# Kernel optimization log

Hardware: AMD Instinct MI355X
Metric: run time of the kernel (lower is better)

The kernel has to match this reference:

```python
import jax, jax.numpy as jnp
import numpy as np
from math import pi

EPS = 1e-7
GAIN = 3.5  # weight_logits_softmax_gain
MAX_LOG_VAR = 3.5


def _upper_triangular(v, T, K, D):
    # replicate tf concat([v, v[...,::-1], zeros[...,D]], axis=2) -> reshape [T,K,D,D] -> strict-upper mask
    zero_pad = jnp.zeros((T, K, D), dtype=v.dtype)
    a_flat = jnp.concatenate([v, v[..., ::-1], zero_pad], axis=2)
    a = a_flat.reshape(T, K, D, D)
    idx = jnp.arange(D)
    mask = (idx[:, None] < idx[None, :]).astype(v.dtype)
    return a * mask[None, None, :, :]


def _diag_transforms(cov_param, T, K, D):
    ut = _upper_triangular(cov_param, T, K, D)
    a = 0.5 * (jnp.swapaxes(ut, -1, -2) - ut)  # antisymmetric [T,K,D,D]
    eye = jnp.eye(D, dtype=cov_param.dtype)[None, None]
    q = jnp.matmul(eye - a, jnp.linalg.inv(eye + a))  # Cayley transform
    return q


def setup_inputs() -> dict:
    key = jax.random.key(0)
    k1, k2, k3, k4, k5 = jax.random.split(key, 5)
    B, T, K, D = 2048, 512, 8, 8
    x = jax.random.normal(k1, (B, T, D), dtype=jnp.float32)
    kernel_centers = jax.random.uniform(k2, (T, K, D), dtype=jnp.float32)
    weight_logits = jax.random.normal(k3, (T, K), dtype=jnp.float32)
    log_variance = jax.random.normal(k4, (T, K, D), dtype=jnp.float32)
    cov_param = jax.random.normal(k5, (T, K, D * (D - 1) // 2), dtype=jnp.float32)
    return {"x": x, "kernel_centers": kernel_centers, "weight_logits": weight_logits,
            "log_variance": log_variance, "cov_param": cov_param}


def reference(x, kernel_centers, weight_logits, log_variance, cov_param):
    T, K, D = kernel_centers.shape
    # subtract kernel centers: [B,T,K,D]
    xc = x[:, :, None, :] - kernel_centers[None]
    # covariance-diagonalizing rotation (Cayley transform of antisym matrix)
    q = _diag_transforms(cov_param, T, K, D)  # [T,K,D,D]
    xt = jnp.einsum('btki,tkij->btkj', xc, q)
    # per-dimension Gaussian pdf
    var = jnp.exp(jnp.clip(log_variance, -MAX_LOG_VAR, MAX_LOG_VAR))[None]  # [1,T,K,D]
    norm_coeff = 1.0 / jnp.sqrt(2.0 * pi * var)
    gaussians = norm_coeff * jnp.exp(-0.5 * xt * xt / var)  # [B,T,K,D]
    # mix: product over dims (in log space), weighted sum over kernels
    lgpe = jnp.sum(jnp.log(gaussians + EPS), axis=-1)  # [B,T,K]
    p_kernels = jnp.exp(lgpe)
    w = jax.nn.softmax(jnp.clip(weight_logits, -GAIN, GAIN), axis=-1)  # [T,K]
    p = jnp.sum(p_kernels * w[None], axis=-1)  # [B,T]
    return p
```

## Files before the change

### kernel.cpp

```cpp
#include <hip/hip_runtime.h>
#include <math.h>

#define TDIM 512
#define KDIM 8
#define DDIM 8
#define BDIM 2048
#define EPSF 1e-7f

#ifndef __has_builtin
#define __has_builtin(x) 0
#endif
#if __has_builtin(__builtin_amdgcn_exp2f)
#define FAST_EXP2(x) __builtin_amdgcn_exp2f(x)
#else
#define FAST_EXP2(x) exp2f(x)
#endif

__global__ __launch_bounds__(512, 4) void pecd_fused(
    const float* __restrict__ x,
    const float* __restrict__ centers,
    const float* __restrict__ wlogits,
    const float* __restrict__ logvar,
    const float* __restrict__ covp,
    float* __restrict__ out)
{
    __shared__ float prm[64 * 80];
    __shared__ float Wl[64];
    __shared__ float xs[64 * 68];

    const int tidx   = (int)threadIdx.x;
    const int t0     = (int)blockIdx.x * 8;
    const int b_base = (int)blockIdx.y * 256;

    {
        const int tk = tidx >> 3;
        const int r  = tidx & 7;
        const int kk = tk & 7;
        const int tl = tk >> 3;
        const size_t tkg = (size_t)(t0 + tl) * 8 + kk;

        const float* cb = covp + tkg * 28;
        float row[8];
        #pragma unroll
        for (int j = 0; j < 8; j++) {
            const int lo = (r < j) ? r : j;
            const int hi = (r < j) ? j : r;
            const int n  = 8 * lo + hi;
            const int m  = (r == j) ? 0 : ((n < 28) ? n : 55 - n);
            const float v = cb[m];
            const float a = (r < j) ? -0.5f * v : 0.5f * v;
            row[j] = (r == j) ? 1.0f : a;
        }

        #pragma unroll
        for (int c = 0; c < 8; c++) {
            float prow[8];
            #pragma unroll
            for (int j = 0; j < 8; j++) prow[j] = __shfl(row[j], c, 8);
            const float pinv = 1.0f / prow[c];
            const float f = row[c];
            #pragma unroll
            for (int j = 0; j < 8; j++) {
                if (j == c) {
                    row[j] = (r == c) ? pinv : -f * pinv;
                } else {
                    const float spiv = prow[j] * pinv;
                    row[j] = (r == c) ? spiv : fmaf(-f, spiv, row[j]);
                }
            }
        }

        const float* lvp = logvar + tkg * 8;
        float invstd[8];
        #pragma unroll
        for (int j = 0; j < 8; j++) {
            const float lv = fminf(fmaxf(lvp[j], -3.5f), 3.5f);
            invstd[j] = exp2f(lv * -0.7213475204444817f);
        }
        const float cr = centers[tkg * 8 + r];
        float* pp = prm + tk * 80;
        float offp[8];
        #pragma unroll
        for (int j = 0; j < 8; j++) {
            const float q = 2.0f * row[j] - (r == j ? 1.0f : 0.0f);
            const float val = q * (invstd[j] * 0.8493218002880191f);
            pp[j * 8 + r] = val;
            offp[j] = cr * val;
        }
        #pragma unroll
        for (int j = 0; j < 8; j++) {
            offp[j] += __shfl_xor(offp[j], 1, 8);
            offp[j] += __shfl_xor(offp[j], 2, 8);
            offp[j] += __shfl_xor(offp[j], 4, 8);
        }
        if (r == 0) {
            #pragma unroll
            for (int j = 0; j < 8; j++) {
                pp[64 + j] = offp[j];
                pp[72 + j] = 0.3989422804014327f * invstd[j];
            }
        }

        float l = fminf(fmaxf(wlogits[tkg], -3.5f), 3.5f);
        float mx = l;
        mx = fmaxf(mx, __shfl_xor(mx, 8, 64));
        mx = fmaxf(mx, __shfl_xor(mx, 16, 64));
        mx = fmaxf(mx, __shfl_xor(mx, 32, 64));
        const float e = exp2f((l - mx) * 1.4426950408889634f);
        float ss = e;
        ss += __shfl_xor(ss, 8, 64);
        ss += __shfl_xor(ss, 16, 64);
        ss += __shfl_xor(ss, 32, 64);
        if (r == 0) Wl[tk] = e / ss;
    }

    const int wave = tidx >> 6;
    const int lane = tidx & 63;

    float xv[4][8];
    #pragma unroll
    for (int c = 0; c < 4; c++) {
        const int b0 = b_base + c * 64;
        __syncthreads();
        #pragma unroll
        for (int it = 0; it < 2; it++) {
            const int idx  = tidx + it * 512;
            const int brow = idx >> 4;
            const int col  = idx & 15;
            const float4 val =
                *((const float4*)(x + ((size_t)(b0 + brow) * TDIM + t0) * DDIM) + col);
            *(float4*)(xs + brow * 68 + col * 4) = val;
        }
        __syncthreads();
        const float* xr = xs + lane * 68 + wave * 8;
        const float4 a0 = *(const float4*)(xr);
        const float4 a1 = *(const float4*)(xr + 4);
        xv[c][0] = a0.x; xv[c][1] = a0.y; xv[c][2] = a0.z; xv[c][3] = a0.w;
        xv[c][4] = a1.x; xv[c][5] = a1.y; xv[c][6] = a1.z; xv[c][7] = a1.w;
    }

    const float* pw = prm + wave * (8 * 80);
    float acc[4] = {0.f, 0.f, 0.f, 0.f};
    #pragma unroll 1
    for (int k = 0; k < KDIM; k++) {
        const float* pk = pw + k * 80;
        float off[8], nc[8];
        *(float4*)&off[0] = *(const float4*)(pk + 64);
        *(float4*)&off[4] = *(const float4*)(pk + 68);
        *(float4*)&nc[0]  = *(const float4*)(pk + 72);
        *(float4*)&nc[4]  = *(const float4*)(pk + 76);
        const float wk = Wl[wave * 8 + k];
        float prod[4] = {1.f, 1.f, 1.f, 1.f};
        #pragma unroll
        for (int j = 0; j < 8; j++) {
            float rr[8];
            *(float4*)&rr[0] = *(const float4*)(pk + j * 8);
            *(float4*)&rr[4] = *(const float4*)(pk + j * 8 + 4);
            #pragma unroll
            for (int c = 0; c < 4; c++) {
                float u = -off[j];
                #pragma unroll
                for (int i = 0; i < 8; i++) u = fmaf(xv[c][i], rr[i], u);
                const float e2 = FAST_EXP2(-(u * u));
                prod[c] *= fmaf(nc[j], e2, EPSF);
            }
        }
        #pragma unroll
        for (int c = 0; c < 4; c++) acc[c] = fmaf(wk, prod[c], acc[c]);
    }

    #pragma unroll
    for (int c = 0; c < 4; c++)
        out[(size_t)(b_base + c * 64 + lane) * TDIM + (t0 + wave)] = acc[c];
}

extern "C" void kernel_launch(void* const* d_in, const int* in_sizes, int n_in,
                              void* d_out, int out_size, void* d_ws, size_t ws_size,
                              hipStream_t stream) {
    const float* x       = (const float*)d_in[0];
    const float* centers = (const float*)d_in[1];
    const float* wlogits = (const float*)d_in[2];
    const float* logvar  = (const float*)d_in[3];
    const float* covp    = (const float*)d_in[4];
    float* out = (float*)d_out;
    (void)d_ws; (void)ws_size;

    dim3 grid(TDIM / 8, BDIM / 256);
    pecd_fused<<<grid, dim3(512), 0, stream>>>(x, centers, wlogits, logvar, covp, out);
}
```

Baseline: 104.0 us.

## Split parameter precompute into separate kernel and fold product into single exp2

Moves the Cayley inverse, variance and softmax setup into a separate precompute kernel that writes per-(t,k) parameters to workspace. The main kernel then reads those parameters with wave-uniform scalar loads. It replaces the product of eight per-dimension Gaussians with one exp2 of a log-domain sum, folding the normalisation and weight into a single constant. Output is staged through shared memory for coalesced stores, and the grid and occupancy are retiled. Dropping EPS inside the log changes the numerics slightly, and the precompute is now redone by a second launch on every call.

After: 100.4 us. -3.5%, faster.

```diff
diff --git a/kernel.cpp b/kernel.cpp
--- a/kernel.cpp
+++ b/kernel.cpp
@@ -5,7 +5,8 @@
 #define KDIM 8
 #define DDIM 8
 #define BDIM 2048
-#define EPSF 1e-7f
+
+#define PSTRIDE 76
 
 #ifndef __has_builtin
 #define __has_builtin(x) 0
@@ -16,162 +17,144 @@
 #define FAST_EXP2(x) exp2f(x)
 #endif
 
-__global__ __launch_bounds__(512, 4) void pecd_fused(
-    const float* __restrict__ x,
+__global__ __launch_bounds__(512) void precompute_kernel(
     const float* __restrict__ centers,
     const float* __restrict__ wlogits,
     const float* __restrict__ logvar,
     const float* __restrict__ covp,
-    float* __restrict__ out)
+    float* __restrict__ P)
 {
-    __shared__ float prm[64 * 80];
-    __shared__ float Wl[64];
-    __shared__ float xs[64 * 68];
+    const int tid = (int)blockIdx.x * 512 + (int)threadIdx.x;
+    const int tk  = tid >> 3;
+    const int r   = tid & 7;
+    const size_t tkg = (size_t)tk;
 
-    const int tidx   = (int)threadIdx.x;
-    const int t0     = (int)blockIdx.x * 8;
-    const int b_base = (int)blockIdx.y * 256;
-
-    {
-        const int tk = tidx >> 3;
-        const int r  = tidx & 7;
-        const int kk = tk & 7;
-        const int tl = tk >> 3;
-        const size_t tkg = (size_t)(t0 + tl) * 8 + kk;
-
-        const float* cb = covp + tkg * 28;
-        float row[8];
-        #pragma unroll
-        for (int j = 0; j < 8; j++) {
-            const int lo = (r < j) ? r : j;
-            const int hi = (r < j) ? j : r;
-            const int n  = 8 * lo + hi;
-            const int m  = (r == j) ? 0 : ((n < 28) ? n : 55 - n);
-            const float v = cb[m];
-            const float a = (r < j) ? -0.5f * v : 0.5f * v;
-            row[j] = (r == j) ? 1.0f : a;
-        }
-
-        #pragma unroll
-        for (int c = 0; c < 8; c++) {
-            float prow[8];
-            #pragma unroll
-            for (int j = 0; j < 8; j++) prow[j] = __shfl(row[j], c, 8);
-            const float pinv = 1.0f / prow[c];
-            const float f = row[c];
-            #pragma unroll
-            for (int j = 0; j < 8; j++) {
-                if (j == c) {
-                    row[j] = (r == c) ? pinv : -f * pinv;
-                } else {
-                    const float spiv = prow[j] * pinv;
-                    row[j] = (r == c) ? spiv : fmaf(-f, spiv, row[j]);
-                }
-            }
-        }
-
-        const float* lvp = logvar + tkg * 8;
-        float invstd[8];
-        #pragma unroll
-        for (int j = 0; j < 8; j++) {
-            const float lv = fminf(fmaxf(lvp[j], -3.5f), 3.5f);
-            invstd[j] = exp2f(lv * -0.7213475204444817f);
-        }
-        const float cr = centers[tkg * 8 + r];
-        float* pp = prm + tk * 80;
-        float offp[8];
-        #pragma unroll
-        for (int j = 0; j < 8; j++) {
-            const float q = 2.0f * row[j] - (r == j ? 1.0f : 0.0f);
-            const float val = q * (invstd[j] * 0.8493218002880191f);
-            pp[j * 8 + r] = val;
-            offp[j] = cr * val;
-        }
-        #pragma unroll
-        for (int j = 0; j < 8; j++) {
-            offp[j] += __shfl_xor(offp[j], 1, 8);
-            offp[j] += __shfl_xor(offp[j], 2, 8);
-            offp[j] += __shfl_xor(offp[j], 4, 8);
-        }
-        if (r == 0) {
-            #pragma unroll
-            for (int j = 0; j < 8; j++) {
-                pp[64 + j] = offp[j];
-                pp[72 + j] = 0.3989422804014327f * invstd[j];
-            }
-        }
-
-        float l = fminf(fmaxf(wlogits[tkg], -3.5f), 3.5f);
-        float mx = l;
-        mx = fmaxf(mx, __shfl_xor(mx, 8, 64));
-        mx = fmaxf(mx, __shfl_xor(mx, 16, 64));
-        mx = fmaxf(mx, __shfl_xor(mx, 32, 64));
-        const float e = exp2f((l - mx) * 1.4426950408889634f);
-        float ss = e;
-        ss += __shfl_xor(ss, 8, 64);
-        ss += __shfl_xor(ss, 16, 64);
-        ss += __shfl_xor(ss, 32, 64);
-        if (r == 0) Wl[tk] = e / ss;
-    }
-
-    const int wave = tidx >> 6;
-    const int lane = tidx & 63;
-
-    float xv[4][8];
+    const float* cb = covp + tkg * 28;
+    float row[8];
     #pragma unroll
-    for (int c = 0; c < 4; c++) {
-        const int b0 = b_base + c * 64;
-        __syncthreads();
-        #pragma unroll
-        for (int it = 0; it < 2; it++) {
-            const int idx  = tidx + it * 512;
-            const int brow = idx >> 4;
-            const int col  = idx & 15;
-            const float4 val =
-                *((const float4*)(x + ((size_t)(b0 + brow) * TDIM + t0) * DDIM) + col);
-            *(float4*)(xs + brow * 68 + col * 4) = val;
-        }
-        __syncthreads();
-        const float* xr = xs + lane * 68 + wave * 8;
-        const float4 a0 = *(const float4*)(xr);
-        const float4 a1 = *(const float4*)(xr + 4);
-        xv[c][0] = a0.x; xv[c][1] = a0.y; xv[c][2] = a0.z; xv[c][3] = a0.w;
-        xv[c][4] = a1.x; xv[c][5] = a1.y; xv[c][6] = a1.z; xv[c][7] = a1.w;
-    }
-
-    const float* pw = prm + wave * (8 * 80);
-    float acc[4] = {0.f, 0.f, 0.f, 0.f};
-    #pragma unroll 1
-    for (int k = 0; k < KDIM; k++) {
-        const float* pk = pw + k * 80;
-        float off[8], nc[8];
-        *(float4*)&off[0] = *(const float4*)(pk + 64);
-        *(float4*)&off[4] = *(const float4*)(pk + 68);
-        *(float4*)&nc[0]  = *(const float4*)(pk + 72);
-        *(float4*)&nc[4]  = *(const float4*)(pk + 76);
-        const float wk = Wl[wave * 8 + k];
-        float prod[4] = {1.f, 1.f, 1.f, 1.f};
-        #pragma unroll
-        for (int j = 0; j < 8; j++) {
-            float rr[8];
-            *(float4*)&rr[0] = *(const float4*)(pk + j * 8);
-            *(float4*)&rr[4] = *(const float4*)(pk + j * 8 + 4);
-            #pragma unroll
-            for (int c = 0; c < 4; c++) {
-                float u = -off[j];
-                #pragma unroll
-                for (int i = 0; i < 8; i++) u = fmaf(xv[c][i], rr[i], u);
-                const float e2 = FAST_EXP2(-(u * u));
-                prod[c] *= fmaf(nc[j], e2, EPSF);
-            }
-        }
-        #pragma unroll
-        for (int c = 0; c < 4; c++) acc[c] = fmaf(wk, prod[c], acc[c]);
+    for (int j = 0; j < 8; j++) {
+        const int lo = (r < j) ? r : j;
+        const int hi = (r < j) ? j : r;
+        const int n  = 8 * lo + hi;
+        const int m  = (r == j) ? 0 : ((n < 28) ? n : 55 - n);
+        const float v = cb[m];
+        const float a = (r < j) ? -0.5f * v : 0.5f * v;
+        row[j] = (r == j) ? 1.0f : a;
     }
 
     #pragma unroll
-    for (int c = 0; c < 4; c++)
-        out[(size_t)(b_base + c * 64 + lane) * TDIM + (t0 + wave)] = acc[c];
+    for (int c = 0; c < 8; c++) {
+        float prow[8];
+        #pragma unroll
+        for (int j = 0; j < 8; j++) prow[j] = __shfl(row[j], c, 8);
+        const float pinv = 1.0f / prow[c];
+        const float f = row[c];
+        #pragma unroll
+        for (int j = 0; j < 8; j++) {
+            if (j == c) {
+                row[j] = (r == c) ? pinv : -f * pinv;
+            } else {
+                const float spiv = prow[j] * pinv;
+                row[j] = (r == c) ? spiv : fmaf(-f, spiv, row[j]);
+            }
+        }
+    }
+
+    const float* lvp = logvar + tkg * 8;
+    float invstd[8];
+    float sumlv = 0.0f;
+    #pragma unroll
+    for (int j = 0; j < 8; j++) {
+        const float lv = fminf(fmaxf(lvp[j], -3.5f), 3.5f);
+        sumlv += lv;
+        invstd[j] = exp2f(lv * -0.7213475204444817f);
+    }
+    const float cr = centers[tkg * 8 + r];
+    float* pp = P + tkg * PSTRIDE;
+    float offp[8];
+    #pragma unroll
+    for (int j = 0; j < 8; j++) {
+        const float q = 2.0f * row[j] - (r == j ? 1.0f : 0.0f);
+        const float val = q * (invstd[j] * 0.8493218002880191f);
+        pp[j * 8 + r] = val;
+        offp[j] = cr * val;
+    }
+    #pragma unroll
+    for (int j = 0; j < 8; j++) {
+        offp[j] += __shfl_xor(offp[j], 1, 8);
+        offp[j] += __shfl_xor(offp[j], 2, 8);
+        offp[j] += __shfl_xor(offp[j], 4, 8);
+    }
+
+    float l = fminf(fmaxf(wlogits[tkg], -3.5f), 3.5f);
+    float mx = l;
+    mx = fmaxf(mx, __shfl_xor(mx, 8, 64));
+    mx = fmaxf(mx, __shfl_xor(mx, 16, 64));
+    mx = fmaxf(mx, __shfl_xor(mx, 32, 64));
+    const float e = exp2f((l - mx) * 1.4426950408889634f);
+    float ss = e;
+    ss += __shfl_xor(ss, 8, 64);
+    ss += __shfl_xor(ss, 16, 64);
+    ss += __shfl_xor(ss, 32, 64);
+    const float log2w = (l - mx) * 1.4426950408889634f - log2f(ss);
+
+    if (r == 0) {
+        #pragma unroll
+        for (int j = 0; j < 8; j++) pp[64 + j] = offp[j];
+        pp[72] = log2w - 10.605984517349169f - 0.7213475204444817f * sumlv;
+    }
+}
+
+__global__ __launch_bounds__(512, 6) void pecd_main(
+    const float* __restrict__ x,
+    const float* __restrict__ P,
+    float* __restrict__ out)
+{
+    __shared__ float os[64 * 18];
+
+    const int tidx = (int)threadIdx.x;
+    const int wv   = tidx >> 6;
+    const int ln   = tidx & 63;
+    const int t0   = (int)blockIdx.x * 16;
+    const int b0   = (int)blockIdx.y * 64;
+
+    const float* xb = x + ((size_t)(b0 + ln) * TDIM + t0) * DDIM;
+
+    #pragma unroll
+    for (int tt = 0; tt < 2; tt++) {
+        const int tl = wv * 2 + tt;
+        const int ts = __builtin_amdgcn_readfirstlane(t0 + tl);
+        const float* __restrict__ pt = P + (size_t)ts * (KDIM * PSTRIDE);
+
+        const float4 a0 = *(const float4*)(xb + tl * 8);
+        const float4 a1 = *(const float4*)(xb + tl * 8 + 4);
+        const float xv[8] = {a0.x, a0.y, a0.z, a0.w, a1.x, a1.y, a1.z, a1.w};
+
+        float acc = 0.0f;
+        #pragma unroll 1
+        for (int k = 0; k < KDIM; k++) {
+            const float* pk = pt + k * PSTRIDE;
+            float s0 = 0.0f, s1 = 0.0f;
+            #pragma unroll
+            for (int j = 0; j < 8; j++) {
+                float u = -pk[64 + j];
+                #pragma unroll
+                for (int i = 0; i < 8; i++) u = fmaf(xv[i], pk[j * 8 + i], u);
+                if (j & 1) s1 = fmaf(u, u, s1);
+                else       s0 = fmaf(u, u, s0);
+            }
+            acc += FAST_EXP2(pk[72] - s0 - s1);
+        }
+        os[ln * 18 + tl] = acc;
+    }
+    __syncthreads();
+
+    {
+        const int row = tidx >> 3;
+        const int col = tidx & 7;
+        const float2 v = *(const float2*)&os[row * 18 + col * 2];
+        *(float2*)(out + (size_t)(b0 + row) * TDIM + t0 + col * 2) = v;
+    }
 }
 
 extern "C" void kernel_launch(void* const* d_in, const int* in_sizes, int n_in,
@@ -183,8 +166,12 @@
     const float* logvar  = (const float*)d_in[3];
     const float* covp    = (const float*)d_in[4];
     float* out = (float*)d_out;
-    (void)d_ws; (void)ws_size;
 
-    dim3 grid(TDIM / 8, BDIM / 256);
-    pecd_fused<<<grid, dim3(512), 0, stream>>>(x, centers, wlogits, logvar, covp, out);
+    float* P = (float*)d_ws;
+
+    precompute_kernel<<<dim3(TDIM * KDIM * 8 / 512), dim3(512), 0, stream>>>(
+        centers, wlogits, logvar, covp, P);
+
+    dim3 grid(TDIM / 16, BDIM / 64);
+    pecd_main<<<grid, dim3(512), 0, stream>>>(x, P, out);
 }
```
